# Performance work log

Hardware: AMD Instinct MI355X
Metric: run time of the kernel (lower is better)

## Reference

```python
import jax, jax.numpy as jnp
import numpy as np

PRIOR_VAR = 0.01
NUM_HEADS = 12
EMBED_DIM = 768


def kl_regularizer(mu, logvar):
    kl_loss = (jnp.log(PRIOR_VAR) - 1.0 - logvar
               + jax.nn.softplus(logvar) / PRIOR_VAR
               + jnp.square(mu) / PRIOR_VAR)
    return 0.5 * jnp.mean(kl_loss)


def linear_vdp(mu_in, Sigma_in, w_mu, w_sigma):
    # mu_in, Sigma_in: [..., Din]; w_mu: [Din, Dout]; w_sigma: [Dout]
    mu_out = mu_in @ w_mu
    kl = kl_regularizer(w_mu, w_sigma)
    W_Sigma = jax.nn.softplus(w_sigma)                      # [Dout]
    din = w_mu.shape[0]
    # w_t_Sigma_i_w: w scaled by sqrt(Din)
    w_scaled = w_mu / jnp.sqrt(jnp.float32(din))
    Sigma_1 = Sigma_in @ (w_scaled * w_scaled)              # [..., Dout]
    # x_Sigma_w_x_T: x scaled by Din
    x = mu_in / jnp.float32(din)
    xx_t = jnp.sum(x * x, axis=-1, keepdims=True)
    Sigma_2 = xx_t * W_Sigma
    # tr_Sigma_w_Sigma_in
    Sigma_3 = jnp.sum(Sigma_in, axis=-1, keepdims=True) * W_Sigma / jnp.float32(w_mu.shape[-1])
    Sigma_out = jax.nn.softplus(Sigma_1 + Sigma_2 + Sigma_3)
    return mu_out, Sigma_out, kl


def split_heads(x, B, H, d):
    # [B, S, E] -> [B, H, S, d]
    return x.reshape(B, -1, H, d).transpose(0, 2, 1, 3)


def vdp_attention(mu_q, sg_q, mu_k, sg_k, mu_v, sg_v):
    d = jnp.float32(mu_k.shape[-1])
    sq = jnp.sqrt(d)
    mu_score = jnp.einsum('bhqd,bhkd->bhqk', mu_q, mu_k)
    a = jnp.einsum('bhqd,bhkd->bhqk', mu_q * mu_q / d, sg_k)
    b = jnp.einsum('bhid,bhjd->bhij', mu_k * mu_k / d, sg_q)  # TF matmul(key.., query.., transpose_b)
    c = jnp.einsum('bhqd,bhkd->bhqk', sg_q / sq, sg_k / sq)
    sigma_score = a + b + c
    mu_weights = jax.nn.softmax(mu_score / sq, axis=-1)
    wdim = jnp.float32(mu_weights.shape[-1])
    grad = jnp.square(mu_weights - mu_weights * mu_weights)
    Sigma_weights = grad * (sigma_score / d) / wdim
    mu_out = jnp.einsum('bhqk,bhkd->bhqd', mu_weights, mu_v)
    dterm = jnp.einsum('bhqk,bhkd->bhqd', mu_weights * mu_weights / wdim, sg_v)
    eterm = jnp.einsum('bhqk,bhkd->bhqd', Sigma_weights, mu_v * mu_v / wdim)
    fterm = jnp.einsum('bhqk,bhkd->bhqd', Sigma_weights / jnp.sqrt(wdim), sg_v / jnp.sqrt(wdim))
    out_sigma = jax.nn.softplus(dterm + eterm + fterm)
    return mu_out, out_sigma


def forward(mu_inputs, sigma_inputs, wq_mu, wq_sigma, wk_mu, wk_sigma,
            wv_mu, wv_sigma, wo_mu, wo_sigma):
    B = mu_inputs.shape[0]
    H = NUM_HEADS
    d = EMBED_DIM // H
    # VDP_Dropout with Training=False is identity
    mu_q, sg_q, kl_q = linear_vdp(mu_inputs, sigma_inputs, wq_mu, wq_sigma)
    mu_k, sg_k, kl_k = linear_vdp(mu_inputs, sigma_inputs, wk_mu, wk_sigma)
    mu_v, sg_v, kl_v = linear_vdp(mu_inputs, sigma_inputs, wv_mu, wv_sigma)
    mu_q, sg_q = split_heads(mu_q, B, H, d), split_heads(sg_q, B, H, d)
    mu_k, sg_k = split_heads(mu_k, B, H, d), split_heads(sg_k, B, H, d)
    mu_v, sg_v = split_heads(mu_v, B, H, d), split_heads(sg_v, B, H, d)
    mu_att, sg_att = vdp_attention(mu_q, sg_q, mu_k, sg_k, mu_v, sg_v)
    mu_cat = mu_att.transpose(0, 2, 1, 3).reshape(B, -1, EMBED_DIM)
    sg_cat = sg_att.transpose(0, 2, 1, 3).reshape(B, -1, EMBED_DIM)
    mu_out, Sigma_out, kl_c = linear_vdp(mu_cat, sg_cat, wo_mu, wo_sigma)
    Sigma_out = jax.nn.softplus(Sigma_out)
    kl = kl_q + kl_k + kl_v + kl_c
    return mu_out, Sigma_out, kl


def setup_inputs() -> dict:
    key = jax.random.key(0)
    ks = jax.random.split(key, 12)
    B, S, E = 4, 1024, EMBED_DIM
    glorot_std = np.sqrt(2.0 / (E + E)).astype(np.float32)
    def wsig(k):
        return jax.random.uniform(k, (E,), jnp.float32, -4.6, -2.25)
    return {
        'mu_inputs': jax.random.normal(ks[0], (B, S, E), jnp.float32),
        'sigma_inputs': jax.random.uniform(ks[1], (B, S, E), jnp.float32),
        'wq_mu': jax.random.normal(ks[2], (E, E), jnp.float32) * glorot_std,
        'wq_sigma': wsig(ks[3]),
        'wk_mu': jax.random.normal(ks[4], (E, E), jnp.float32) * glorot_std,
        'wk_sigma': wsig(ks[5]),
        'wv_mu': jax.random.normal(ks[6], (E, E), jnp.float32) * glorot_std,
        'wv_sigma': wsig(ks[7]),
        'wo_mu': jax.random.normal(ks[8], (E, E), jnp.float32) * glorot_std,
        'wo_sigma': wsig(ks[9]),
    }


def reference(mu_inputs, sigma_inputs, wq_mu, wq_sigma, wk_mu, wk_sigma,
              wv_mu, wv_sigma, wo_mu, wo_sigma):
    return forward(mu_inputs, sigma_inputs, wq_mu, wq_sigma, wk_mu, wk_sigma,
                   wv_mu, wv_sigma, wo_mu, wo_sigma)
```

## Files before the change

kernel.cpp:

```cpp
#include <hip/hip_runtime.h>
#include <math.h>

#define E 768
#define NTOK 4096

typedef __attribute__((ext_vector_type(8))) __bf16 bf16x8;
typedef __attribute__((ext_vector_type(4))) float f32x4;
typedef unsigned int u32;
typedef unsigned short u16;
typedef __attribute__((ext_vector_type(4))) u32 u32x4;

#define BFN ((size_t)NTOK * E)
#define WFN ((size_t)E * E)
#define QSC 1.4901161193847656e-08f
#define C2E 0.18033688011112042f

__device__ __forceinline__ float sp_f(float x) {
    return fmaxf(x, 0.f) + log1pf(__expf(-fabsf(x)));
}
__device__ __forceinline__ u16 f2bf(float f) {
    u32 u = __float_as_uint(f);
    u += 0x7fffu + ((u >> 16) & 1u);
    return (u16)(u >> 16);
}
__device__ __forceinline__ u32 pk2(float a, float b) {
    return (u32)f2bf(a) | ((u32)f2bf(b) << 16);
}
__device__ __forceinline__ u32 cvtpk(float a, float b) {
    u32 r; asm("v_cvt_pk_bf16_f32 %0, %1, %2" : "=v"(r) : "v"(a), "v"(b)); return r;
}
__device__ __forceinline__ float ex2(float x) {
    float r; asm("v_exp_f32 %0, %1" : "=v"(r) : "v"(x)); return r;
}
__device__ __forceinline__ float lg2(float x) {
    float r; asm("v_log_f32 %0, %1" : "=v"(r) : "v"(x)); return r;
}
__device__ __forceinline__ float bfl(u32 u) { return __uint_as_float(u << 16); }
__device__ __forceinline__ float bfh(u32 u) { return __uint_as_float(u & 0xffff0000u); }

#define GLL16(gp, lp) __builtin_amdgcn_global_load_lds( \
    (const __attribute__((address_space(1))) u32*)(gp), \
    (__attribute__((address_space(3))) u32*)(lp), 16, 0, 0)

#define SBAR() do { __builtin_amdgcn_sched_barrier(0); \
                    __builtin_amdgcn_s_barrier(); \
                    __builtin_amdgcn_sched_barrier(0); } while (0)
#define VMCNT(N) do { asm volatile("s_waitcnt vmcnt(" #N ")" ::: "memory"); \
                      __builtin_amdgcn_sched_barrier(0); } while (0)

__global__ __launch_bounds__(256) void prep_all(
    const float* __restrict__ mu_in, const float* __restrict__ sg_in,
    const float* __restrict__ wq, const float* __restrict__ wk,
    const float* __restrict__ wvp, const float* __restrict__ wo,
    const float* __restrict__ wqs, const float* __restrict__ wks,
    const float* __restrict__ wvs, const float* __restrict__ wos,
    u16* __restrict__ Xmu, u16* __restrict__ Xsg,
    float* __restrict__ rmu2, float* __restrict__ rsg,
    u16* __restrict__ WtAll, u16* __restrict__ W2tAll,
    float* __restrict__ spws, float* __restrict__ kl_out)
{
    __shared__ float T[32][33];
    __shared__ float r1[4], r2[4];
    const int b = blockIdx.x, tid = threadIdx.x;

    if (b < 2048) {
        const int half = tid >> 7;
        const int n = b * 2 + half;
        const int t2 = tid & 127;
        float s1 = 0.f, s2 = 0.f;
        if (t2 < 96) {
            size_t o = (size_t)n * E + t2 * 8;
            float4 a0 = *(const float4*)(mu_in + o), a1 = *(const float4*)(mu_in + o + 4);
            float4 b0 = *(const float4*)(sg_in + o), b1 = *(const float4*)(sg_in + o + 4);
            *(uint4*)(Xmu + o) = make_uint4(pk2(a0.x, a0.y), pk2(a0.z, a0.w), pk2(a1.x, a1.y), pk2(a1.z, a1.w));
            *(uint4*)(Xsg + o) = make_uint4(pk2(b0.x, b0.y), pk2(b0.z, b0.w), pk2(b1.x, b1.y), pk2(b1.z, b1.w));
            s1 = a0.x*a0.x + a0.y*a0.y + a0.z*a0.z + a0.w*a0.w + a1.x*a1.x + a1.y*a1.y + a1.z*a1.z + a1.w*a1.w;
            s2 = b0.x + b0.y + b0.z + b0.w + b1.x + b1.y + b1.z + b1.w;
        }
        for (int off = 32; off; off >>= 1) {
            s1 += __shfl_xor(s1, off);
            s2 += __shfl_xor(s2, off);
        }
        if ((tid & 63) == 0) { r1[tid >> 6] = s1; r2[tid >> 6] = s2; }
        __syncthreads();
        if (t2 == 0) {
            rmu2[n] = r1[half * 2] + r1[half * 2 + 1];
            rsg[n]  = r2[half * 2] + r2[half * 2 + 1];
        }
    } else if (b < 4352) {
        const int b2 = b - 2048;
        const int z = b2 / 576, rem = b2 - z * 576;
        const float* W = (z == 0) ? wq : (z == 1) ? wk : (z == 2) ? wvp : wo;
        u16* Wt  = WtAll  + (size_t)z * WFN;
        u16* W2t = W2tAll + (size_t)z * WFN;
        const int j0 = (rem % 24) * 32, k0 = (rem / 24) * 32;
        const int r = tid >> 3, c = (tid & 7) * 4;
        float4 v = *(const float4*)(W + (size_t)(k0 + r) * E + j0 + c);
        T[r][c] = v.x; T[r][c + 1] = v.y; T[r][c + 2] = v.z; T[r][c + 3] = v.w;
        __syncthreads();
        const int j = tid >> 3, kc = (tid & 7) * 4;
        float w0 = T[kc][j], w1 = T[kc + 1][j], w2 = T[kc + 2][j], w3 = T[kc + 3][j];
        size_t o = (size_t)(j0 + j) * E + k0 + kc;
        *(uint2*)(Wt + o) = make_uint2(pk2(w0, w1), pk2(w2, w3));
        const float s = 1.f / 768.f;
        *(uint2*)(W2t + o) = make_uint2(pk2(w0 * w0 * s, w1 * w1 * s), pk2(w2 * w2 * s, w3 * w3 * s));
    } else if (b < 4864) {
        const int gid = (b - 4352) * 256 + tid;
        const int gsz = 512 * 256;
        float acc = 0.f;
        const float cw = 100.f / ((float)E * (float)E);
#pragma unroll
        for (int mm = 0; mm < 4; ++mm) {
            const float* w  = (mm == 0) ? wq  : (mm == 1) ? wk  : (mm == 2) ? wvp : wo;
            const float* sv = (mm == 0) ? wqs : (mm == 1) ? wks : (mm == 2) ? wvs : wos;
            for (int i = gid; i < E * E; i += gsz) { float x = w[i]; acc += x * x * cw; }
            for (int i = gid; i < E; i += gsz) { float x = sv[i]; acc += (-x + sp_f(x) * 100.f) * (1.f / (float)E); }
        }
        if (b == 4352 && tid == 0) acc += 4.f * (logf(0.01f) - 1.f);
        for (int off = 32; off; off >>= 1) acc += __shfl_xor(acc, off);
        if ((tid & 63) == 0) r1[tid >> 6] = acc;
        __syncthreads();
        if (tid == 0) atomicAdd(kl_out, 0.5f * (r1[0] + r1[1] + r1[2] + r1[3]));
    } else {
        for (int i = tid; i < 4 * E; i += 256) {
            const float* src;
            int j;
            if (i < E)            { src = wqs; j = i; }
            else if (i < 2 * E)   { src = wks; j = i - E; }
            else if (i < 3 * E)   { src = wvs; j = i - 2 * E; }
            else                  { src = wos; j = i - 3 * E; }
            spws[i] = sp_f(src[j]);
        }
    }
}

__global__ __launch_bounds__(128) void rowstats_bf16_kernel(
    const u16* __restrict__ mu, const u16* __restrict__ sg,
    float* __restrict__ rmu2, float* __restrict__ rsg)
{
    const int n = blockIdx.x, tid = threadIdx.x;
    float s1 = 0.f, s2 = 0.f;
    if (tid < 96) {
        uint4 um = *(const uint4*)(mu + (size_t)n * E + tid * 8);
        uint4 us = *(const uint4*)(sg + (size_t)n * E + tid * 8);
        u32 ua[4] = {um.x, um.y, um.z, um.w};
        u32 ub[4] = {us.x, us.y, us.z, us.w};
#pragma unroll
        for (int j = 0; j < 4; ++j) {
            float a0 = bfl(ua[j]), a1 = bfh(ua[j]);
            s1 += a0 * a0 + a1 * a1;
            s2 += bfl(ub[j]) + bfh(ub[j]);
        }
    }
    for (int off = 32; off; off >>= 1) {
        s1 += __shfl_xor(s1, off);
        s2 += __shfl_xor(s2, off);
    }
    __shared__ float r1[2], r2[2];
    if ((tid & 63) == 0) { r1[tid >> 6] = s1; r2[tid >> 6] = s2; }
    __syncthreads();
    if (tid == 0) { rmu2[n] = r1[0] + r1[1]; rsg[n] = r2[0] + r2[1]; }
}

template<int MODE>
__global__ __launch_bounds__(256, 3) void linear_fused(
    const u16* __restrict__ Am, const u16* __restrict__ As,
    const u16* __restrict__ Wt, const u16* __restrict__ W2t,
    const float* __restrict__ spws, const float* __restrict__ rmu2, const float* __restrict__ rsg,
    float* __restrict__ mu_out, float* __restrict__ sg_out, u16* __restrict__ QKVB)
{
    __shared__ __align__(16) u16 L[24576];

    const int wgid = blockIdx.x;
    const int NW = (MODE == 1) ? 144 : 48;
    const int NB = (MODE == 1) ? 36 : 12;
    const int swz = (wgid & 7) * NW + (wgid >> 3);
    const int m_blk = swz / NB, n_blk = swz % NB;
    const int m0 = m_blk * 128, col0 = n_blk * 64;
    const int tid = threadIdx.x, wv = tid >> 6, lane = tid & 63;
    const int g = lane >> 4, q15 = lane & 15;

    const u16* sp_[6];
    {
        const int rA = tid >> 2, cA = tid & 3;
        const int rB = 64 + rA;
        const int csA = (cA ^ ((rA >> 1) & 3)) << 3;
        const int csB = (cA ^ ((rB >> 1) & 3)) << 3;
        sp_[0] = Am  + (size_t)(m0 + rA) * E + csA;
        sp_[1] = Am  + (size_t)(m0 + rB) * E + csB;
        sp_[2] = As  + (size_t)(m0 + rA) * E + csA;
        sp_[3] = As  + (size_t)(m0 + rB) * E + csB;
        sp_[4] = Wt  + (size_t)(col0 + rA) * E + csA;
        sp_[5] = W2t + (size_t)(col0 + rA) * E + csA;
    }

    f32x4 acc1[2][4], acc2[2][4];
#pragma unroll
    for (int mt = 0; mt < 2; ++mt)
#pragma unroll
        for (int nt = 0; nt < 4; ++nt) {
            acc1[mt][nt] = (f32x4){0.f, 0.f, 0.f, 0.f};
            acc2[mt][nt] = (f32x4){0.f, 0.f, 0.f, 0.f};
        }

#pragma unroll
    for (int j = 0; j < 6; ++j)
        GLL16(sp_[j], &L[j * 2048 + tid * 8]);

    for (int t = 0; t < 24; ++t) {
        SBAR();
        const int tn = (t < 23) ? t + 1 : 23;
        const int nb = ((t & 1) ^ 1) * 12288;
#pragma unroll
        for (int j = 0; j < 6; ++j)
            GLL16(sp_[j] + tn * 32, &L[nb + j * 2048 + tid * 8]);
        VMCNT(6);
        SBAR();
        const int cb = (t & 1) * 12288;
        bf16x8 am[2], asg[2];
#pragma unroll
        for (int mt = 0; mt < 2; ++mt) {
            int r = wv * 32 + mt * 16 + q15;
            int c = (g ^ ((r >> 1) & 3)) << 3;
            am[mt]  = *(const bf16x8*)&L[cb + r * 32 + c];
            asg[mt] = *(const bf16x8*)&L[cb + 4096 + r * 32 + c];
        }
        __builtin_amdgcn_s_setprio(1);
#pragma unroll
        for (int nt = 0; nt < 4; ++nt) {
            int rb = nt * 16 + q15;
            int c = (g ^ ((rb >> 1) & 3)) << 3;
            bf16x8 bw = *(const bf16x8*)&L[cb + 8192 + rb * 32 + c];
            bf16x8 b2 = *(const bf16x8*)&L[cb + 10240 + rb * 32 + c];
            acc1[0][nt] = __builtin_amdgcn_mfma_f32_16x16x32_bf16(am[0], bw, acc1[0][nt], 0, 0, 0);
            acc1[1][nt] = __builtin_amdgcn_mfma_f32_16x16x32_bf16(am[1], bw, acc1[1][nt], 0, 0, 0);
            acc2[0][nt] = __builtin_amdgcn_mfma_f32_16x16x32_bf16(asg[0], b2, acc2[0][nt], 0, 0, 0);
            acc2[1][nt] = __builtin_amdgcn_mfma_f32_16x16x32_bf16(asg[1], b2, acc2[1][nt], 0, 0, 0);
        }
        __builtin_amdgcn_s_setprio(0);
    }
    __syncthreads();

    const float inv2 = 1.f / (768.f * 768.f), invd = 1.f / 768.f;
    float rr[2][4];
#pragma unroll
    for (int mt = 0; mt < 2; ++mt)
#pragma unroll
        for (int r = 0; r < 4; ++r) {
            int row = m0 + wv * 32 + mt * 16 + g * 4 + r;
            rr[mt][r] = rmu2[row] * inv2 + rsg[row] * invd;
        }

    if (MODE == 0) {
#pragma unroll
        for (int mt = 0; mt < 2; ++mt)
#pragma unroll
            for (int nt = 0; nt < 4; ++nt)
#pragma unroll
                for (int r = 0; r < 4; ++r) {
                    int row = m0 + wv * 32 + mt * 16 + g * 4 + r;
                    int col = col0 + nt * 16 + q15;
                    float mu = acc1[mt][nt][r];
                    float sg = sp_f(sp_f(acc2[mt][nt][r] + rr[mt][r] * spws[col]));
                    mu_out[(size_t)row * E + col] = mu;
                    sg_out[(size_t)row * E + col] = sg;
                }
    } else {
        const int proj = n_blk / 12, h = n_blk % 12;
        if (proj < 2) {
            u16* b0 = QKVB + (size_t)(proj * 3 + 0) * BFN;
            u16* b1 = QKVB + (size_t)(proj * 3 + 1) * BFN;
            u16* b2 = QKVB + (size_t)(proj * 3 + 2) * BFN;
#pragma unroll
            for (int mt = 0; mt < 2; ++mt)
#pragma unroll
                for (int nt = 0; nt < 4; ++nt)
#pragma unroll
                    for (int r = 0; r < 4; ++r) {
                        int row = m0 + wv * 32 + mt * 16 + g * 4 + r;
                        int col = col0 + nt * 16 + q15;
                        float mu = acc1[mt][nt][r];
                        float sg = sp_f(acc2[mt][nt][r] + rr[mt][r] * spws[col]);
                        int bb = row >> 10, s = row & 1023, d = nt * 16 + q15;
                        size_t rb = ((size_t)(bb * 12 + h) << 16) + ((size_t)s << 6) + d;
                        b0[rb] = f2bf(mu);
                        b1[rb] = f2bf(sg);
                        b2[rb] = f2bf(proj == 0 ? (mu * mu + sg) * QSC : mu * mu * QSC);
                    }
        } else {
            float sgv[2][4][4];
#pragma unroll
            for (int mt = 0; mt < 2; ++mt)
#pragma unroll
                for (int nt = 0; nt < 4; ++nt)
#pragma unroll
                    for (int r = 0; r < 4; ++r) {
                        int col = col0 + nt * 16 + q15;
                        sgv[mt][nt][r] = sp_f(acc2[mt][nt][r] + rr[mt][r] * spws[col]);
                    }
            const int bb = m0 >> 10, s0 = m0 & 1023;
#pragma unroll
            for (int a = 0; a < 3; ++a) {
                __syncthreads();
#pragma unroll
                for (int mt = 0; mt < 2; ++mt)
#pragma unroll
                    for (int nt = 0; nt < 4; ++nt)
#pragma unroll
                        for (int r = 0; r < 4; ++r) {
                            float mu = acc1[mt][nt][r], sg = sgv[mt][nt][r];
                            float v = (a == 0) ? mu : (a == 1) ? sg * 0.0009765625f : mu * mu + sg;
                            L[(nt * 16 + q15) * 136 + wv * 32 + g * 8 + mt * 4 + r] = f2bf(v);
                        }
                __syncthreads();
                const int d = tid >> 2, sc = (tid & 3) * 32;
                u16* dst = QKVB + (size_t)(6 + a) * BFN;
                size_t ga = ((size_t)((bb * 12 + h) * 64 + d) << 10) + s0 + sc;
                *(uint4*)(dst + ga)      = *(const uint4*)&L[d * 136 + sc];
                *(uint4*)(dst + ga + 8)  = *(const uint4*)&L[d * 136 + sc + 8];
                *(uint4*)(dst + ga + 16) = *(const uint4*)&L[d * 136 + sc + 16];
                *(uint4*)(dst + ga + 24) = *(const uint4*)&L[d * 136 + sc + 24];
            }
        }
    }
}

#define KB0 0
#define KB1 6144
#define VB  12288
__global__ __launch_bounds__(256, 3) void vdp_attn7(
    const u16* __restrict__ Kmu, const u16* __restrict__ Ksg, const u16* __restrict__ Asq,
    const u16* __restrict__ Qmu, const u16* __restrict__ Q1v, const u16* __restrict__ Q2v,
    const u16* __restrict__ Vmu, const u16* __restrict__ Vsg, const u16* __restrict__ Vw2,
    u16* __restrict__ om, u16* __restrict__ osg)
{
    __shared__ __align__(16) u16 L[18432];

    const int wgid = blockIdx.x;
    const int seq = (wgid & 7) * 96 + (wgid >> 3);
    const int bh = seq >> 4, qt = seq & 15;
    const int tid = threadIdx.x, wv = tid >> 6, lane = tid & 63;
    const int g = lane >> 4, q15 = lane & 15;
    const size_t hb = (size_t)bh << 16;

    const size_t qoff = hb + (size_t)((qt * 64 + wv * 16 + q15) << 6) + g * 8;
    bf16x8 bq0 = *(const bf16x8*)(Qmu + qoff), bq1 = *(const bf16x8*)(Qmu + qoff + 32);
    bf16x8 b10 = *(const bf16x8*)(Q1v + qoff), b11 = *(const bf16x8*)(Q1v + qoff + 32);
    bf16x8 b20 = *(const bf16x8*)(Q2v + qoff), b21 = *(const bf16x8*)(Q2v + qoff + 32);

    const int sr = tid >> 3, sc8 = tid & 7;
    const size_t koffA = hb + (size_t)sr * 64 + ((sc8 ^ (sr & 7)) << 3);
    const size_t koffB = hb + (size_t)(sr + 32) * 64 + ((sc8 ^ (sr & 7)) << 3);
    const int vr = tid >> 2, vc = tid & 3;
    const size_t voff = hb + (size_t)vr * 1024 + ((vc ^ ((vr >> 1) & 3)) << 3);

    float m2 = -3.0e38f;
    float lacc[4] = {0.f, 0.f, 0.f, 0.f};
    GLL16(Kmu + koffA, &L[0 + wv * 512]);
    GLL16(Kmu + koffB, &L[2048 + wv * 512]);
    __syncthreads();
    for (int t = 0; t < 16; ++t) {
        SBAR();
        const int tn = (t < 15) ? t + 1 : 15;
        const int nb = (t & 1) ? 0 : 4096;
        GLL16(Kmu + koffA + ((size_t)tn << 12), &L[nb + wv * 512]);
        GLL16(Kmu + koffB + ((size_t)tn << 12), &L[nb + 2048 + wv * 512]);
        VMCNT(2);
        SBAR();
        const int kb = (t & 1) ? 4096 : 0;
        f32x4 sc[4];
#pragma unroll
        for (int kt = 0; kt < 4; ++kt) sc[kt] = (f32x4){0.f, 0.f, 0.f, 0.f};
        __builtin_amdgcn_s_setprio(1);
#pragma unroll
        for (int kt = 0; kt < 4; ++kt) {
            int row = kt * 16 + q15, ra = kb + (row << 6);
            bf16x8 k0 = *(const bf16x8*)&L[ra + ((g ^ (row & 7)) << 3)];
            bf16x8 k1 = *(const bf16x8*)&L[ra + (((g + 4) ^ (row & 7)) << 3)];
            sc[kt] = __builtin_amdgcn_mfma_f32_16x16x32_bf16(k0, bq0, sc[kt], 0, 0, 0);
            sc[kt] = __builtin_amdgcn_mfma_f32_16x16x32_bf16(k1, bq1, sc[kt], 0, 0, 0);
        }
        __builtin_amdgcn_s_setprio(0);
        float t0 = fmaxf(fmaxf(sc[0][0], sc[0][1]), fmaxf(sc[0][2], sc[0][3]));
        float t1 = fmaxf(fmaxf(sc[1][0], sc[1][1]), fmaxf(sc[1][2], sc[1][3]));
        float t2 = fmaxf(fmaxf(sc[2][0], sc[2][1]), fmaxf(sc[2][2], sc[2][3]));
        float t3 = fmaxf(fmaxf(sc[3][0], sc[3][1]), fmaxf(sc[3][2], sc[3][3]));
        float tm = fmaxf(fmaxf(t0, t1), fmaxf(t2, t3)) * C2E;
        if (tm > m2 + 8.f) {
            float f = ex2(m2 - tm);
            lacc[0] *= f; lacc[1] *= f; lacc[2] *= f; lacc[3] *= f;
            m2 = tm;
        }
#pragma unroll
        for (int kt = 0; kt < 4; ++kt)
#pragma unroll
            for (int r = 0; r < 4; ++r)
                lacc[kt] += ex2(fmaf(sc[kt][r], C2E, -m2));
    }
    __syncthreads();
    float l = (lacc[0] + lacc[1]) + (lacc[2] + lacc[3]);
#pragma unroll
    for (int off = 16; off <= 32; off <<= 1) {
        float mo = __shfl_xor(m2, off), lo = __shfl_xor(l, off);
        float nm = fmaxf(m2, mo);
        l = l * ex2(m2 - nm) + lo * ex2(mo - nm);
        m2 = nm;
    }
    const float M = m2 + lg2(l);

    f32x4 accm[4], accd[4], acce[4];
#pragma unroll
    for (int nt = 0; nt < 4; ++nt) {
        accm[nt] = (f32x4){0.f, 0.f, 0.f, 0.f};
        accd[nt] = (f32x4){0.f, 0.f, 0.f, 0.f};
        acce[nt] = (f32x4){0.f, 0.f, 0.f, 0.f};
    }

    int cur = 0;
    GLL16(Kmu + koffA, &L[KB0 + 0    + wv * 512]);
    GLL16(Ksg + koffA, &L[KB0 + 2048 + wv * 512]);
    GLL16(Asq + koffA, &L[KB0 + 4096 + wv * 512]);
    __syncthreads();

    for (int t = 0; t < 32; ++t) {
        SBAR();
        const size_t va = (size_t)t << 5;
        GLL16(Vmu + voff + va, &L[VB + 0    + wv * 512]);
        GLL16(Vsg + voff + va, &L[VB + 2048 + wv * 512]);
        GLL16(Vw2 + voff + va, &L[VB + 4096 + wv * 512]);
        const int tn = (t < 31) ? t + 1 : 31;
        const size_t ka = (size_t)tn << 11;
        const int nb = cur ? KB0 : KB1;
        GLL16(Kmu + koffA + ka, &L[nb + 0    + wv * 512]);
        GLL16(Ksg + koffA + ka, &L[nb + 2048 + wv * 512]);
        GLL16(Asq + koffA + ka, &L[nb + 4096 + wv * 512]);
        VMCNT(6);
        SBAR();

        const int kb = cur ? KB1 : KB0;
        f32x4 sc[2], sgc[2];
#pragma unroll
        for (int kt = 0; kt < 2; ++kt) { sc[kt] = (f32x4){0.f,0.f,0.f,0.f}; sgc[kt] = (f32x4){0.f,0.f,0.f,0.f}; }
        __builtin_amdgcn_s_setprio(1);
#pragma unroll
        for (int kt = 0; kt < 2; ++kt) {
            int row = kt * 16 + q15, ra = kb + (row << 6);
            int ca = ((g ^ (row & 7)) << 3), cb = (((g + 4) ^ (row & 7)) << 3);
            sc[kt]  = __builtin_amdgcn_mfma_f32_16x16x32_bf16(*(const bf16x8*)&L[ra + ca],        bq0, sc[kt],  0, 0, 0);
            sc[kt]  = __builtin_amdgcn_mfma_f32_16x16x32_bf16(*(const bf16x8*)&L[ra + cb],        bq1, sc[kt],  0, 0, 0);
            sgc[kt] = __builtin_amdgcn_mfma_f32_16x16x32_bf16(*(const bf16x8*)&L[2048 + ra + ca], b10, sgc[kt], 0, 0, 0);
            sgc[kt] = __builtin_amdgcn_mfma_f32_16x16x32_bf16(*(const bf16x8*)&L[2048 + ra + cb], b11, sgc[kt], 0, 0, 0);
            sgc[kt] = __builtin_amdgcn_mfma_f32_16x16x32_bf16(*(const bf16x8*)&L[4096 + ra + ca], b20, sgc[kt], 0, 0, 0);
            sgc[kt] = __builtin_amdgcn_mfma_f32_16x16x32_bf16(*(const bf16x8*)&L[4096 + ra + cb], b21, sgc[kt], 0, 0, 0);
        }
        __builtin_amdgcn_s_setprio(0);

        float p[8], p2v[8], swv[8];
#pragma unroll
        for (int kt = 0; kt < 2; ++kt)
#pragma unroll
            for (int r = 0; r < 4; ++r) {
                int j = kt * 4 + r;
                float pv = ex2(fmaf(sc[kt][r], C2E, -M));
                float pp = pv * pv;
                float gq = pv - pp;
                p[j] = pv; p2v[j] = pp; swv[j] = gq * gq * sgc[kt][r];
            }
        u32x4 ua = {cvtpk(p[0], p[1]),   cvtpk(p[2], p[3]),   cvtpk(p[4], p[5]),   cvtpk(p[6], p[7])};
        u32x4 ub = {cvtpk(p2v[0], p2v[1]), cvtpk(p2v[2], p2v[3]), cvtpk(p2v[4], p2v[5]), cvtpk(p2v[6], p2v[7])};
        u32x4 uc = {cvtpk(swv[0], swv[1]), cvtpk(swv[2], swv[3]), cvtpk(swv[4], swv[5]), cvtpk(swv[6], swv[7])};
        bf16x8 pa  = *(const bf16x8*)&ua;
        bf16x8 p2a = *(const bf16x8*)&ub;
        bf16x8 swa = *(const bf16x8*)&uc;

        VMCNT(3);
        SBAR();

        __builtin_amdgcn_s_setprio(1);
#pragma unroll
        for (int nt = 0; nt < 4; ++nt) {
            int row = nt * 16 + q15;
            int vi = (row << 5) + ((g ^ ((q15 >> 1) & 3)) << 3);
            accm[nt] = __builtin_amdgcn_mfma_f32_16x16x32_bf16(pa,  *(const bf16x8*)&L[VB + vi],        accm[nt], 0, 0, 0);
            accd[nt] = __builtin_amdgcn_mfma_f32_16x16x32_bf16(p2a, *(const bf16x8*)&L[VB + 2048 + vi], accd[nt], 0, 0, 0);
            acce[nt] = __builtin_amdgcn_mfma_f32_16x16x32_bf16(swa, *(const bf16x8*)&L[VB + 4096 + vi], acce[nt], 0, 0, 0);
        }
        __builtin_amdgcn_s_setprio(0);
        cur ^= 1;
    }

    const int b_ = bh / 12, h_ = bh % 12;
#pragma unroll
    for (int nt = 0; nt < 4; ++nt)
#pragma unroll
        for (int r = 0; r < 4; ++r) {
            int srow = qt * 64 + wv * 16 + g * 4 + r;
            int d = nt * 16 + q15;
            size_t o = (size_t)(b_ * 1024 + srow) * E + h_ * 64 + d;
            om[o]  = f2bf(accm[nt][r]);
            osg[o] = f2bf(sp_f(accd[nt][r] + acce[nt][r]));
        }
}

extern "C" void kernel_launch(void* const* d_in, const int* in_sizes, int n_in,
                              void* d_out, int out_size, void* d_ws, size_t ws_size,
                              hipStream_t stream)
{
    const float* mu_in = (const float*)d_in[0];
    const float* sg_in = (const float*)d_in[1];
    const float* wq  = (const float*)d_in[2];
    const float* wqs = (const float*)d_in[3];
    const float* wk  = (const float*)d_in[4];
    const float* wks = (const float*)d_in[5];
    const float* wvp = (const float*)d_in[6];
    const float* wvs = (const float*)d_in[7];
    const float* wo  = (const float*)d_in[8];
    const float* wos = (const float*)d_in[9];

    float* out_mu = (float*)d_out;
    float* out_sg = out_mu + (size_t)NTOK * E;
    float* kl_out = out_mu + 2 * (size_t)NTOK * E;

    float* ws = (float*)d_ws;
    size_t off = 0;
    auto allocf = [&](size_t n) { float* p = ws + off; off += n; return p; };
    float* rmu2  = allocf(NTOK);
    float* rsgs  = allocf(NTOK);
    float* armu2 = allocf(NTOK);
    float* arsg  = allocf(NTOK);
    float* spws  = allocf(4 * E);

    u16* ub = (u16*)(ws + off);
    size_t uoff = 0;
    auto allocu = [&](size_t n) { u16* p = ub + uoff; uoff += n; return p; };
    u16* Xmu    = allocu(BFN);
    u16* Xsg    = allocu(BFN);
    u16* WtAll  = allocu(4 * WFN);
    u16* W2tAll = allocu(4 * WFN);
    u16* QKVB   = allocu(9 * BFN);
    u16* amu_b  = allocu(BFN);
    u16* asg_b  = allocu(BFN);
    (void)ws_size; (void)in_sizes; (void)n_in; (void)out_size;

    hipMemsetAsync(kl_out, 0, 4, stream);
    prep_all<<<4865, 256, 0, stream>>>(mu_in, sg_in, wq, wk, wvp, wo,
                                       wqs, wks, wvs, wos,
                                       Xmu, Xsg, rmu2, rsgs, WtAll, W2tAll,
                                       spws, kl_out);

    linear_fused<1><<<1152, 256, 0, stream>>>(Xmu, Xsg, WtAll, W2tAll, spws, rmu2, rsgs,
                                              nullptr, nullptr, QKVB);

    vdp_attn7<<<768, 256, 0, stream>>>(QKVB + 3 * BFN, QKVB + 4 * BFN, QKVB + 1 * BFN,
                                       QKVB + 0 * BFN, QKVB + 2 * BFN, QKVB + 5 * BFN,
                                       QKVB + 6 * BFN, QKVB + 7 * BFN, QKVB + 8 * BFN,
                                       amu_b, asg_b);

    rowstats_bf16_kernel<<<NTOK, 128, 0, stream>>>(amu_b, asg_b, armu2, arsg);
    linear_fused<0><<<384, 256, 0, stream>>>(amu_b, asg_b, WtAll + 3 * WFN, W2tAll + 3 * WFN,
                                             spws + 3 * E, armu2, arsg,
                                             out_mu, out_sg, nullptr);
}
```

Measured before the change: 226.0 us.

## Double-buffer V tiles in attention, stage Q/K epilogue through LDS, remap tile grid

The attention kernel now double-buffers the V tiles alongside K and prefetches the next V tile together with the next K tile. This removes the second wait-and-barrier inside each iteration, at the cost of more LDS per block (48KB). The QKV projection epilogue for Q and K now goes through shared memory so it can issue 16-byte vectorized global stores instead of scattered 2-byte stores. The workgroup-to-tile mapping changes so each XCD handles a contiguous group of M blocks, which is meant to improve L2 reuse of the activation rows. The larger LDS footprint may lower occupancy.

```diff
diff --git a/kernel.cpp b/kernel.cpp
--- a/kernel.cpp
+++ b/kernel.cpp
@@ -172,10 +172,9 @@
     __shared__ __align__(16) u16 L[24576];
 
     const int wgid = blockIdx.x;
-    const int NW = (MODE == 1) ? 144 : 48;
-    const int NB = (MODE == 1) ? 36 : 12;
-    const int swz = (wgid & 7) * NW + (wgid >> 3);
-    const int m_blk = swz / NB, n_blk = swz % NB;
+    const int xcd = wgid & 7, local = wgid >> 3;
+    const int m_blk = xcd * 4 + (local & 3);
+    const int n_blk = local >> 2;
     const int m0 = m_blk * 128, col0 = n_blk * 64;
     const int tid = threadIdx.x, wv = tid >> 6, lane = tid & 63;
     const int g = lane >> 4, q15 = lane & 15;
@@ -267,38 +266,43 @@
                 }
     } else {
         const int proj = n_blk / 12, h = n_blk % 12;
+        float sgv[2][4][4];
+#pragma unroll
+        for (int mt = 0; mt < 2; ++mt)
+#pragma unroll
+            for (int nt = 0; nt < 4; ++nt)
+#pragma unroll
+                for (int r = 0; r < 4; ++r) {
+                    int col = col0 + nt * 16 + q15;
+                    sgv[mt][nt][r] = sp_f(acc2[mt][nt][r] + rr[mt][r] * spws[col]);
+                }
+        const int bb = m0 >> 10;
         if (proj < 2) {
-            u16* b0 = QKVB + (size_t)(proj * 3 + 0) * BFN;
-            u16* b1 = QKVB + (size_t)(proj * 3 + 1) * BFN;
-            u16* b2 = QKVB + (size_t)(proj * 3 + 2) * BFN;
-#pragma unroll
-            for (int mt = 0; mt < 2; ++mt)
-#pragma unroll
-                for (int nt = 0; nt < 4; ++nt)
-#pragma unroll
-                    for (int r = 0; r < 4; ++r) {
-                        int row = m0 + wv * 32 + mt * 16 + g * 4 + r;
-                        int col = col0 + nt * 16 + q15;
-                        float mu = acc1[mt][nt][r];
-                        float sg = sp_f(acc2[mt][nt][r] + rr[mt][r] * spws[col]);
-                        int bb = row >> 10, s = row & 1023, d = nt * 16 + q15;
-                        size_t rb = ((size_t)(bb * 12 + h) << 16) + ((size_t)s << 6) + d;
-                        b0[rb] = f2bf(mu);
-                        b1[rb] = f2bf(sg);
-                        b2[rb] = f2bf(proj == 0 ? (mu * mu + sg) * QSC : mu * mu * QSC);
-                    }
+            const int s0 = (m0 & 1023);
+            const int sl = tid >> 1, hh = tid & 1;
+            size_t gbase = ((size_t)(bb * 12 + h) << 16) + ((size_t)(s0 + sl) << 6) + hh * 32;
+#pragma unroll
+            for (int a = 0; a < 3; ++a) {
+                __syncthreads();
+#pragma unroll
+                for (int mt = 0; mt < 2; ++mt)
+#pragma unroll
+                    for (int nt = 0; nt < 4; ++nt)
+#pragma unroll
+                        for (int r = 0; r < 4; ++r) {
+                            float mu = acc1[mt][nt][r], sg = sgv[mt][nt][r];
+                            float v = (a == 0) ? mu : (a == 1) ? sg :
+                                      (proj == 0 ? (mu * mu + sg) * QSC : mu * mu * QSC);
+                            L[(wv * 32 + mt * 16 + g * 4 + r) * 72 + nt * 16 + q15] = f2bf(v);
+                        }
+                __syncthreads();
+                u16* dst = QKVB + (size_t)(proj * 3 + a) * BFN;
+#pragma unroll
+                for (int j = 0; j < 4; ++j)
+                    *(uint4*)(dst + gbase + j * 8) = *(const uint4*)&L[sl * 72 + hh * 32 + j * 8];
+            }
         } else {
-            float sgv[2][4][4];
-#pragma unroll
-            for (int mt = 0; mt < 2; ++mt)
-#pragma unroll
-                for (int nt = 0; nt < 4; ++nt)
-#pragma unroll
-                    for (int r = 0; r < 4; ++r) {
-                        int col = col0 + nt * 16 + q15;
-                        sgv[mt][nt][r] = sp_f(acc2[mt][nt][r] + rr[mt][r] * spws[col]);
-                    }
-            const int bb = m0 >> 10, s0 = m0 & 1023;
+            const int s0 = m0 & 1023;
 #pragma unroll
             for (int a = 0; a < 3; ++a) {
                 __syncthreads();
@@ -327,14 +331,15 @@
 
 #define KB0 0
 #define KB1 6144
-#define VB  12288
-__global__ __launch_bounds__(256, 3) void vdp_attn7(
+#define VB0 12288
+#define VB1 18432
+__global__ __launch_bounds__(256, 3) void vdp_attn8(
     const u16* __restrict__ Kmu, const u16* __restrict__ Ksg, const u16* __restrict__ Asq,
     const u16* __restrict__ Qmu, const u16* __restrict__ Q1v, const u16* __restrict__ Q2v,
     const u16* __restrict__ Vmu, const u16* __restrict__ Vsg, const u16* __restrict__ Vw2,
     u16* __restrict__ om, u16* __restrict__ osg)
 {
-    __shared__ __align__(16) u16 L[18432];
+    __shared__ __align__(16) u16 L[24576];
 
     const int wgid = blockIdx.x;
     const int seq = (wgid & 7) * 96 + (wgid >> 3);
@@ -416,28 +421,32 @@
         acce[nt] = (f32x4){0.f, 0.f, 0.f, 0.f};
     }
 
-    int cur = 0;
     GLL16(Kmu + koffA, &L[KB0 + 0    + wv * 512]);
     GLL16(Ksg + koffA, &L[KB0 + 2048 + wv * 512]);
     GLL16(Asq + koffA, &L[KB0 + 4096 + wv * 512]);
+    GLL16(Vmu + voff, &L[VB0 + 0    + wv * 512]);
+    GLL16(Vsg + voff, &L[VB0 + 2048 + wv * 512]);
+    GLL16(Vw2 + voff, &L[VB0 + 4096 + wv * 512]);
     __syncthreads();
 
     for (int t = 0; t < 32; ++t) {
         SBAR();
-        const size_t va = (size_t)t << 5;
-        GLL16(Vmu + voff + va, &L[VB + 0    + wv * 512]);
-        GLL16(Vsg + voff + va, &L[VB + 2048 + wv * 512]);
-        GLL16(Vw2 + voff + va, &L[VB + 4096 + wv * 512]);
         const int tn = (t < 31) ? t + 1 : 31;
         const size_t ka = (size_t)tn << 11;
-        const int nb = cur ? KB0 : KB1;
-        GLL16(Kmu + koffA + ka, &L[nb + 0    + wv * 512]);
-        GLL16(Ksg + koffA + ka, &L[nb + 2048 + wv * 512]);
-        GLL16(Asq + koffA + ka, &L[nb + 4096 + wv * 512]);
+        const size_t va = (size_t)tn << 5;
+        const int nbK = (t & 1) ? KB0 : KB1;
+        const int nbV = (t & 1) ? VB0 : VB1;
+        GLL16(Kmu + koffA + ka, &L[nbK + 0    + wv * 512]);
+        GLL16(Ksg + koffA + ka, &L[nbK + 2048 + wv * 512]);
+        GLL16(Asq + koffA + ka, &L[nbK + 4096 + wv * 512]);
+        GLL16(Vmu + voff + va,  &L[nbV + 0    + wv * 512]);
+        GLL16(Vsg + voff + va,  &L[nbV + 2048 + wv * 512]);
+        GLL16(Vw2 + voff + va,  &L[nbV + 4096 + wv * 512]);
         VMCNT(6);
         SBAR();
 
-        const int kb = cur ? KB1 : KB0;
+        const int kb = (t & 1) ? KB1 : KB0;
+        const int vb = (t & 1) ? VB1 : VB0;
         f32x4 sc[2], sgc[2];
 #pragma unroll
         for (int kt = 0; kt < 2; ++kt) { sc[kt] = (f32x4){0.f,0.f,0.f,0.f}; sgc[kt] = (f32x4){0.f,0.f,0.f,0.f}; }
@@ -466,27 +475,23 @@
                 float gq = pv - pp;
                 p[j] = pv; p2v[j] = pp; swv[j] = gq * gq * sgc[kt][r];
             }
-        u32x4 ua = {cvtpk(p[0], p[1]),   cvtpk(p[2], p[3]),   cvtpk(p[4], p[5]),   cvtpk(p[6], p[7])};
-        u32x4 ub = {cvtpk(p2v[0], p2v[1]), cvtpk(p2v[2], p2v[3]), cvtpk(p2v[4], p2v[5]), cvtpk(p2v[6], p2v[7])};
-        u32x4 uc = {cvtpk(swv[0], swv[1]), cvtpk(swv[2], swv[3]), cvtpk(swv[4], swv[5]), cvtpk(swv[6], swv[7])};
+        u32x4 ua  = {cvtpk(p[0], p[1]),     cvtpk(p[2], p[3]),     cvtpk(p[4], p[5]),     cvtpk(p[6], p[7])};
+        u32x4 ubv = {cvtpk(p2v[0], p2v[1]), cvtpk(p2v[2], p2v[3]), cvtpk(p2v[4], p2v[5]), cvtpk(p2v[6], p2v[7])};
+        u32x4 ucv = {cvtpk(swv[0], swv[1]), cvtpk(swv[2], swv[3]), cvtpk(swv[4], swv[5]), cvtpk(swv[6], swv[7])};
         bf16x8 pa  = *(const bf16x8*)&ua;
-        bf16x8 p2a = *(const bf16x8*)&ub;
-        bf16x8 swa = *(const bf16x8*)&uc;
-
-        VMCNT(3);
-        SBAR();
+        bf16x8 p2a = *(const bf16x8*)&ubv;
+        bf16x8 swa = *(const bf16x8*)&ucv;
 
         __builtin_amdgcn_s_setprio(1);
 #pragma unroll
         for (int nt = 0; nt < 4; ++nt) {
             int row = nt * 16 + q15;
-            int vi = (row << 5) + ((g ^ ((q15 >> 1) & 3)) << 3);
-            accm[nt] = __builtin_amdgcn_mfma_f32_16x16x32_bf16(pa,  *(const bf16x8*)&L[VB + vi],        accm[nt], 0, 0, 0);
-            accd[nt] = __builtin_amdgcn_mfma_f32_16x16x32_bf16(p2a, *(const bf16x8*)&L[VB + 2048 + vi], accd[nt], 0, 0, 0);
-            acce[nt] = __builtin_amdgcn_mfma_f32_16x16x32_bf16(swa, *(const bf16x8*)&L[VB + 4096 + vi], acce[nt], 0, 0, 0);
+            int vi = vb + (row << 5) + ((g ^ ((q15 >> 1) & 3)) << 3);
+            accm[nt] = __builtin_amdgcn_mfma_f32_16x16x32_bf16(pa,  *(const bf16x8*)&L[vi],        accm[nt], 0, 0, 0);
+            accd[nt] = __builtin_amdgcn_mfma_f32_16x16x32_bf16(p2a, *(const bf16x8*)&L[vi + 2048], accd[nt], 0, 0, 0);
+            acce[nt] = __builtin_amdgcn_mfma_f32_16x16x32_bf16(swa, *(const bf16x8*)&L[vi + 4096], acce[nt], 0, 0, 0);
         }
         __builtin_amdgcn_s_setprio(0);
-        cur ^= 1;
     }
 
     const int b_ = bh / 12, h_ = bh % 12;
@@ -551,7 +556,7 @@
     linear_fused<1><<<1152, 256, 0, stream>>>(Xmu, Xsg, WtAll, W2tAll, spws, rmu2, rsgs,
                                               nullptr, nullptr, QKVB);
 
-    vdp_attn7<<<768, 256, 0, stream>>>(QKVB + 3 * BFN, QKVB + 4 * BFN, QKVB + 1 * BFN,
+    vdp_attn8<<<768, 256, 0, stream>>>(QKVB + 3 * BFN, QKVB + 4 * BFN, QKVB + 1 * BFN,
                                        QKVB + 0 * BFN, QKVB + 2 * BFN, QKVB + 5 * BFN,
                                        QKVB + 6 * BFN, QKVB + 7 * BFN, QKVB + 8 * BFN,
                                        amu_b, asg_b);
```

New measurement: 223.3 us. Within noise of the previous version (-1.2%).
